# Optimization experiments

Measured on AMD Instinct MI355X. Metric: run time of the kernel, lower is better.

Reference implementation:

```python
import jax, jax.numpy as jnp
import numpy as np

B, N, D_IN = 8, 1024, 512
H, D_HEAD = 8, 64
D_EXPAND, D_OUT = 2048, 512
D_Q = D_HEAD * H            # 512
D_V = D_IN * H              # 4096
D_QKV = 2 * D_Q + D_V       # 5120
EPS = 1e-5


def setup_inputs() -> dict:
    key = jax.random.key(0)
    ks = jax.random.split(key, 16)
    s = 0.02
    return {
        "x": jax.random.normal(ks[0], (B, N, D_IN), jnp.float32),
        "pos_enc": jax.random.normal(ks[1], (1, N, D_IN), jnp.float32),
        "gamma1": jnp.ones((1, 1, D_IN), jnp.float32),
        "beta1": jnp.zeros((1, 1, D_IN), jnp.float32),
        "scale": jnp.asarray(1.414, jnp.float32),
        "W_qkv": jax.random.normal(ks[2], (D_IN, D_QKV), jnp.float32) * s,
        "b_qkv": jax.random.normal(ks[3], (D_QKV,), jnp.float32) * s,
        "W_merge": jax.random.normal(ks[4], (D_V, D_IN), jnp.float32) * s,
        "b_merge": jax.random.normal(ks[5], (D_IN,), jnp.float32) * s,
        "gamma2": jnp.ones((1, 1, D_IN), jnp.float32),
        "beta2": jnp.zeros((1, 1, D_IN), jnp.float32),
        "W1": jax.random.normal(ks[6], (D_IN, D_EXPAND), jnp.float32) * s,
        "b1": jax.random.normal(ks[7], (D_EXPAND,), jnp.float32) * s,
        "gamma3": jnp.ones((1, 1, D_EXPAND), jnp.float32),
        "beta3": jnp.zeros((1, 1, D_EXPAND), jnp.float32),
        "W2": jax.random.normal(ks[8], (D_EXPAND, D_OUT), jnp.float32) * s,
        "b2": jax.random.normal(ks[9], (D_OUT,), jnp.float32) * s,
    }


def _feature_norm(x, gamma, beta):
    # torch FeatureNorm: stats over dim=1 (sequence dim), unbiased=False
    mean = x.mean(axis=1, keepdims=True)
    var = x.var(axis=1, keepdims=True)
    return gamma * (x - mean) / jnp.sqrt(var + EPS) + beta


def _swish(x):
    return x * jax.nn.sigmoid(x)


def reference(x, pos_enc, gamma1, beta1, scale, W_qkv, b_qkv, W_merge, b_merge,
              gamma2, beta2, W1, b1, gamma3, beta3, W2, b2):
    Bs, Ns, _ = x.shape
    h = _feature_norm(x, gamma1, beta1) + pos_enc
    qkv = _swish(h) @ W_qkv + b_qkv                      # (B, N, D_QKV)
    q = qkv[..., :D_Q].reshape(Bs, Ns, H, D_HEAD).transpose(0, 2, 1, 3)        # (B,H,N,dh)
    k = qkv[..., D_Q:2 * D_Q].reshape(Bs, Ns, H, D_HEAD).transpose(0, 2, 1, 3)
    v = qkv[..., 2 * D_Q:].reshape(Bs, Ns, H, D_IN).transpose(0, 2, 1, 3)      # (B,H,N,d_in)
    # squared euclidean distance via |q|^2 + |k|^2 - 2 q.k
    q2 = jnp.sum(q * q, axis=-1)                         # (B,H,N)
    k2 = jnp.sum(k * k, axis=-1)                         # (B,H,N)
    qk = jnp.einsum('bhnc,bhmc->bhnm', q, k)             # (B,H,N,N)
    d2 = jnp.maximum(q2[..., :, None] + k2[..., None, :] - 2.0 * qk, 0.0)
    score = jnp.exp(-d2 / (scale * scale))               # RBF kernel, no softmax
    out = jnp.einsum('bhnm,bhmc->bhnc', score, v)        # (B,H,N,d_in)
    out = out.transpose(0, 2, 1, 3).reshape(Bs, Ns, H * D_IN)
    x2 = x + out @ W_merge + b_merge                     # merge heads + residual
    ffh = _feature_norm(x2, gamma2, beta2) @ W1 + b1
    ffh = _swish(_feature_norm(ffh, gamma3, beta3))
    ff = ffh @ W2 + b2
    return ff + x2                                        # shortcut is Identity (d_in == d_out)
```

## Files before the change

### kernel.cpp

```cpp
#include <hip/hip_runtime.h>
#include <hip/hip_bf16.h>
#include <stdint.h>

typedef __bf16 bf16_t;
typedef __bf16 bf16x8 __attribute__((ext_vector_type(8)));
typedef __bf16 bf16x4 __attribute__((ext_vector_type(4)));
typedef float f32x4 __attribute__((ext_vector_type(4)));

__global__ void transp_kernel(const float* __restrict__ in, bf16_t* __restrict__ out,
                              int K, int N) {
  __shared__ float tile[32][33];
  int k0 = blockIdx.x * 32, n0 = blockIdx.y * 32;
  int tx = threadIdx.x, ty = threadIdx.y;
#pragma unroll
  for (int i = 0; i < 4; i++)
    tile[ty + 8 * i][tx] = in[(size_t)(k0 + ty + 8 * i) * N + n0 + tx];
  __syncthreads();
#pragma unroll
  for (int i = 0; i < 4; i++)
    out[(size_t)(n0 + ty + 8 * i) * K + k0 + tx] = (bf16_t)tile[tx][ty + 8 * i];
}

#define NSPLIT 16

__global__ __launch_bounds__(256) void norm_partial(
    const float* __restrict__ in, float* __restrict__ part, int D) {
  const int nd = D >> 7;
  const int bid = blockIdx.x;
  const int s = bid % NSPLIT;
  const int rem = bid / NSPLIT;
  const int dc = rem % nd;
  const int b = rem / nd;
  const int t = threadIdx.x;
  const int d = (dc << 7) + (t & 127);
  const int half = t >> 7;
  const int rows = 1024 / NSPLIT;
  const float* base = in + ((size_t)b * 1024 + s * rows) * D + d;
  float sum = 0.f, sq = 0.f;
  for (int n = half; n < rows; n += 2) {
    float v = base[(size_t)n * D];
    sum += v;
    sq += v * v;
  }
  __shared__ float r0[256], r1[256];
  r0[t] = sum;
  r1[t] = sq;
  __syncthreads();
  if (t < 128) {
    float ssum = r0[t] + r0[t + 128];
    float ssq = r1[t] + r1[t + 128];
    size_t col = (size_t)b * D + (dc << 7) + t;
    part[col * (2 * NSPLIT) + s] = ssum;
    part[col * (2 * NSPLIT) + NSPLIT + s] = ssq;
  }
}

__global__ __launch_bounds__(256) void norm_stats(
    const float* __restrict__ part, float2* __restrict__ stats, int total) {
  int col = blockIdx.x * 256 + threadIdx.x;
  if (col >= total) return;
  const float* p = part + (size_t)col * (2 * NSPLIT);
  float sum = 0.f, sq = 0.f;
#pragma unroll
  for (int s = 0; s < NSPLIT; s++) {
    sum += p[s];
    sq += p[NSPLIT + s];
  }
  float mean = sum * (1.f / 1024.f);
  float var = sq * (1.f / 1024.f) - mean * mean;
  stats[col] = make_float2(mean, rsqrtf(var + 1e-5f));
}

template <int MODE>
__global__ __launch_bounds__(256) void norm_apply(
    const float* __restrict__ in, const float2* __restrict__ stats,
    const float* __restrict__ gamma, const float* __restrict__ beta,
    const float* __restrict__ pos, bf16_t* __restrict__ out, int logD) {
  const int D = 1 << logD;
  size_t idx = ((size_t)blockIdx.x * 256 + threadIdx.x) * 4;
  int d = (int)(idx & (D - 1));
  size_t row = idx >> logD;
  int b = (int)(row >> 10);
  int n = (int)(row & 1023);
  float4 v = *(const float4*)(in + idx);
  float4 g = *(const float4*)(gamma + d);
  float4 be = *(const float4*)(beta + d);
  const float2* st = stats + (size_t)b * D + d;
  float vv[4] = {v.x, v.y, v.z, v.w};
  float gg[4] = {g.x, g.y, g.z, g.w};
  float bb[4] = {be.x, be.y, be.z, be.w};
  float pp[4] = {0.f, 0.f, 0.f, 0.f};
  if (MODE == 1) {
    float4 p = *(const float4*)(pos + (size_t)n * D + d);
    pp[0] = p.x; pp[1] = p.y; pp[2] = p.z; pp[3] = p.w;
  }
  bf16x4 o;
#pragma unroll
  for (int j = 0; j < 4; j++) {
    float2 s = st[j];
    float h = gg[j] * (vv[j] - s.x) * s.y + bb[j];
    if (MODE == 1) h += pp[j];
    if (MODE == 1 || MODE == 3) h = h / (1.f + __expf(-h));
    o[j] = (bf16_t)h;
  }
  *(bf16x4*)(out + idx) = o;
}

enum { EPI_QKV = 0, EPI_F32 = 1, EPI_F32RES = 2 };

template <int EPI>
__global__ void __launch_bounds__(256, 2) gemm_bf16(
    const bf16_t* __restrict__ A, const bf16_t* __restrict__ Bt,
    const float* __restrict__ bias, const float* __restrict__ res,
    void* __restrict__ out0, bf16_t* __restrict__ out1,
    int M, int N, int K) {
  __shared__ bf16_t smem[2 * 128 * 64];
  bf16_t* sA = smem;
  bf16_t* sB = smem + 128 * 64;
  const int mt = M >> 7;
  const int bm = blockIdx.x % mt;
  const int bn = blockIdx.x / mt;
  const int t = threadIdx.x;
  const int w = t >> 6, l = t & 63;
  const int wm = w >> 1, wn = w & 1;
  const int lrow = l >> 3;
  const int lcol = (l & 7) ^ lrow;

  f32x4 acc[4][4];
  const f32x4 z4 = {0.f, 0.f, 0.f, 0.f};
#pragma unroll
  for (int m = 0; m < 4; m++)
#pragma unroll
    for (int n = 0; n < 4; n++) acc[m][n] = z4;

  const bf16_t* Asrc = A + (size_t)(bm * 128 + w * 32 + lrow) * K + lcol * 8;
  const bf16_t* Bsrc = Bt + (size_t)(bn * 128 + w * 32 + lrow) * K + lcol * 8;

  for (int kk = 0; kk < K; kk += 64) {
#pragma unroll
    for (int i = 0; i < 4; i++) {
      __builtin_amdgcn_global_load_lds(
          (const __attribute__((address_space(1))) void*)(const void*)(Asrc + (size_t)i * 8 * K + kk),
          (__attribute__((address_space(3))) void*)(void*)((char*)sA + (w * 4 + i) * 1024),
          16, 0, 0);
      __builtin_amdgcn_global_load_lds(
          (const __attribute__((address_space(1))) void*)(const void*)(Bsrc + (size_t)i * 8 * K + kk),
          (__attribute__((address_space(3))) void*)(void*)((char*)sB + (w * 4 + i) * 1024),
          16, 0, 0);
    }
    __syncthreads();
#pragma unroll
    for (int ks = 0; ks < 2; ks++) {
      bf16x8 af[4], bfr[4];
      const int lc = ks * 4 + (l >> 4);
#pragma unroll
      for (int m = 0; m < 4; m++) {
        int row = wm * 64 + m * 16 + (l & 15);
        af[m] = *(const bf16x8*)((const char*)sA + row * 128 + ((lc ^ (row & 7)) << 4));
      }
#pragma unroll
      for (int n = 0; n < 4; n++) {
        int row = wn * 64 + n * 16 + (l & 15);
        bfr[n] = *(const bf16x8*)((const char*)sB + row * 128 + ((lc ^ (row & 7)) << 4));
      }
#pragma unroll
      for (int m = 0; m < 4; m++)
#pragma unroll
        for (int n = 0; n < 4; n++)
          acc[m][n] = __builtin_amdgcn_mfma_f32_16x16x32_bf16(af[m], bfr[n], acc[m][n], 0, 0, 0);
    }
    __syncthreads();
  }

  const int rowbase = bm * 128 + wm * 64 + ((l >> 4) << 2);
  const int colbase = bn * 128 + wn * 64 + (l & 15);
#pragma unroll
  for (int m = 0; m < 4; m++) {
#pragma unroll
    for (int n = 0; n < 4; n++) {
      int row = rowbase + m * 16;
      int col = colbase + n * 16;
      float bc = bias[col];
      if (EPI == EPI_QKV) {
        if (col < 1024) {
          bf16_t* qkb = (bf16_t*)out0;
#pragma unroll
          for (int r = 0; r < 4; r++)
            qkb[(size_t)(row + r) * 1024 + col] = (bf16_t)(acc[m][n][r] + bc);
        } else {
          int c2 = col - 1024;
          int hh = c2 >> 9, vc = c2 & 511;
          int bidx = row >> 10, nidx = row & 1023;
          bf16x4 pk;
#pragma unroll
          for (int r = 0; r < 4; r++) pk[r] = (bf16_t)(acc[m][n][r] + bc);
          *(bf16x4*)(out1 + ((size_t)((bidx << 3) + hh) * 512 + vc) * 1024 + nidx) = pk;
        }
      } else {
        float* o = (float*)out0;
#pragma unroll
        for (int r = 0; r < 4; r++) {
          float v = acc[m][n][r] + bc;
          if (EPI == EPI_F32RES) v += res[(size_t)(row + r) * N + col];
          o[(size_t)(row + r) * N + col] = v;
        }
      }
    }
  }
}

__global__ void q2k2_kernel(const bf16_t* __restrict__ qk, float* __restrict__ q2,
                            float* __restrict__ k2) {
  int tid = blockIdx.x * 256 + threadIdx.x;
  int b = tid >> 13;
  int h = (tid >> 10) & 7;
  int n = tid & 1023;
  const bf16_t* row = qk + (size_t)((b << 10) + n) * 1024 + (h << 6);
  float sq = 0.f, sk = 0.f;
#pragma unroll
  for (int i = 0; i < 8; i++) {
    bf16x8 vq = *(const bf16x8*)(row + i * 8);
    bf16x8 vk = *(const bf16x8*)(row + 512 + i * 8);
#pragma unroll
    for (int j = 0; j < 8; j++) {
      float fq = (float)vq[j];
      sq += fq * fq;
      float fk = (float)vk[j];
      sk += fk * fk;
    }
  }
  q2[tid] = sq;
  k2[tid] = sk;
}

__global__ void __launch_bounds__(256, 2) attn_kernel(
    const bf16_t* __restrict__ qk, const bf16_t* __restrict__ vt,
    const float* __restrict__ q2, const float* __restrict__ k2,
    const float* __restrict__ scale_p, bf16_t* __restrict__ attn_out) {
  __shared__ bf16_t s_lds[64 * 64];
  const int blk = blockIdx.x;
  const int mtile = blk & 15;
  const int bh = blk >> 4;
  const int b = bh >> 3, h = bh & 7;
  const int t = threadIdx.x, w = t >> 6, l = t & 63;
  const float sc = scale_p[0];
  const float minus_inv = -1.f / (sc * sc);

  const bf16_t* qbase = qk + ((size_t)((b << 10) + (mtile << 6))) * 1024 + (h << 6);
  bf16x8 qf[4][2];
#pragma unroll
  for (int it = 0; it < 4; it++)
#pragma unroll
    for (int kc = 0; kc < 2; kc++)
      qf[it][kc] = *(const bf16x8*)(qbase + (size_t)(it * 16 + (l & 15)) * 1024 +
                                    kc * 32 + ((l >> 4) << 3));
  float q2r[4];
  const float* q2base = q2 + (bh << 10) + (mtile << 6);
#pragma unroll
  for (int it = 0; it < 4; it++) q2r[it] = q2base[it * 16 + (l & 15)];

  f32x4 acc[4][8];
  const f32x4 z4 = {0.f, 0.f, 0.f, 0.f};
#pragma unroll
  for (int m = 0; m < 4; m++)
#pragma unroll
    for (int nn = 0; nn < 8; nn++) acc[m][nn] = z4;

  const bf16_t* kbase = qk + ((size_t)(b << 10)) * 1024 + 512 + (h << 6);
  const bf16_t* vbase = vt + ((size_t)(bh << 9)) * 1024;
  const float* k2base = k2 + (bh << 10);

  for (int kt = 0; kt < 16; kt++) {
    float k2r[4];
#pragma unroll
    for (int r = 0; r < 4; r++)
      k2r[r] = k2base[kt * 64 + w * 16 + ((l >> 4) << 2) + r];
    f32x4 sacc[4];
#pragma unroll
    for (int it = 0; it < 4; it++) sacc[it] = z4;
#pragma unroll
    for (int kc = 0; kc < 2; kc++) {
      bf16x8 kf = *(const bf16x8*)(kbase + (size_t)(kt * 64 + w * 16 + (l & 15)) * 1024 +
                                   kc * 32 + ((l >> 4) << 3));
#pragma unroll
      for (int it = 0; it < 4; it++)
        sacc[it] = __builtin_amdgcn_mfma_f32_16x16x32_bf16(kf, qf[it][kc], sacc[it], 0, 0, 0);
    }
    __syncthreads();
#pragma unroll
    for (int it = 0; it < 4; it++) {
      int i = it * 16 + (l & 15);
      bf16x4 pk;
#pragma unroll
      for (int r = 0; r < 4; r++) {
        float d2 = fmaxf(q2r[it] + k2r[r] - 2.f * sacc[it][r], 0.f);
        pk[r] = (bf16_t)__expf(d2 * minus_inv);
      }
      int jc8 = (w << 2) + (l >> 4);
      *(bf16x4*)((char*)s_lds + i * 128 + ((jc8 ^ ((i & 7) << 1)) << 3)) = pk;
    }
    __syncthreads();
#pragma unroll
    for (int kc = 0; kc < 2; kc++) {
      bf16x8 sf[4];
#pragma unroll
      for (int m = 0; m < 4; m++) {
        int i = m * 16 + (l & 15);
        int jcA = (kc << 3) + ((l >> 4) << 1);
        sf[m] = *(const bf16x8*)((const char*)s_lds + i * 128 +
                                 ((jcA ^ ((i & 7) << 1)) << 3));
      }
#pragma unroll
      for (int nn = 0; nn < 8; nn++) {
        bf16x8 vf = *(const bf16x8*)(vbase + (size_t)(w * 128 + nn * 16 + (l & 15)) * 1024 +
                                     kt * 64 + (kc << 5) + ((l >> 4) << 3));
#pragma unroll
        for (int m = 0; m < 4; m++)
          acc[m][nn] = __builtin_amdgcn_mfma_f32_16x16x32_bf16(sf[m], vf, acc[m][nn], 0, 0, 0);
      }
    }
  }
#pragma unroll
  for (int m = 0; m < 4; m++) {
    int nidx = (mtile << 6) + m * 16 + ((l >> 4) << 2);
#pragma unroll
    for (int nn = 0; nn < 8; nn++) {
      int col = (h << 9) + w * 128 + nn * 16 + (l & 15);
      bf16_t* o = attn_out + ((size_t)((b << 10) + nidx)) * 4096 + col;
#pragma unroll
      for (int r = 0; r < 4; r++) o[(size_t)r * 4096] = (bf16_t)acc[m][nn][r];
    }
  }
}

extern "C" void kernel_launch(void* const* d_in, const int* in_sizes, int n_in,
                              void* d_out, int out_size, void* d_ws, size_t ws_size,
                              hipStream_t stream) {
  const float* x    = (const float*)d_in[0];
  const float* pos  = (const float*)d_in[1];
  const float* g1   = (const float*)d_in[2];
  const float* be1  = (const float*)d_in[3];
  const float* scl  = (const float*)d_in[4];
  const float* Wqkv = (const float*)d_in[5];
  const float* bqkv = (const float*)d_in[6];
  const float* Wmrg = (const float*)d_in[7];
  const float* bmrg = (const float*)d_in[8];
  const float* g2   = (const float*)d_in[9];
  const float* be2  = (const float*)d_in[10];
  const float* W1   = (const float*)d_in[11];
  const float* b1   = (const float*)d_in[12];
  const float* g3   = (const float*)d_in[13];
  const float* be3  = (const float*)d_in[14];
  const float* W2   = (const float*)d_in[15];
  const float* b2   = (const float*)d_in[16];
  float* outp = (float*)d_out;

  char* ws = (char*)d_ws;
  size_t off = 0;
  auto alloc = [&](size_t bytes) {
    char* p = ws + off;
    off += (bytes + 255) & ~(size_t)255;
    return p;
  };
  bf16_t* wtq = (bf16_t*)alloc(5120ull * 512 * 2);
  bf16_t* wtm = (bf16_t*)alloc(512ull * 4096 * 2);
  bf16_t* wt1 = (bf16_t*)alloc(2048ull * 512 * 2);
  bf16_t* wt2 = (bf16_t*)alloc(512ull * 2048 * 2);
  float*  q2  = (float*)alloc(65536ull * 4);
  float*  k2  = (float*)alloc(65536ull * 4);
  float*  prt = (float*)alloc(16384ull * 2 * NSPLIT * 4);
  float2* sts = (float2*)alloc(16384ull * 8);
  bf16_t* swh = (bf16_t*)alloc(8192ull * 512 * 2);
  bf16_t* qkb = (bf16_t*)alloc(8192ull * 1024 * 2);
  float*  x2b = (float*)alloc(8192ull * 512 * 4);
  bf16_t* x2n = (bf16_t*)alloc(8192ull * 512 * 2);
  bf16_t* atn = (bf16_t*)alloc(8192ull * 4096 * 2);
  bf16_t* vtb = (bf16_t*)alloc(64ull * 512 * 1024 * 2);
  float*  ffh = (float*)vtb;
  bf16_t* ffn = (bf16_t*)atn;

  dim3 tb(32, 8);
  transp_kernel<<<dim3(512 / 32, 5120 / 32), tb, 0, stream>>>(Wqkv, wtq, 512, 5120);
  transp_kernel<<<dim3(4096 / 32, 512 / 32), tb, 0, stream>>>(Wmrg, wtm, 4096, 512);
  transp_kernel<<<dim3(512 / 32, 2048 / 32), tb, 0, stream>>>(W1, wt1, 512, 2048);
  transp_kernel<<<dim3(2048 / 32, 512 / 32), tb, 0, stream>>>(W2, wt2, 2048, 512);

  norm_partial<<<8 * 4 * NSPLIT, 256, 0, stream>>>(x, prt, 512);
  norm_stats<<<16, 256, 0, stream>>>(prt, sts, 8 * 512);
  norm_apply<1><<<4096, 256, 0, stream>>>(x, sts, g1, be1, pos, swh, 9);

  gemm_bf16<EPI_QKV><<<64 * 40, 256, 0, stream>>>(swh, wtq, bqkv, nullptr,
                                                  (void*)qkb, vtb, 8192, 5120, 512);
  q2k2_kernel<<<256, 256, 0, stream>>>(qkb, q2, k2);
  attn_kernel<<<1024, 256, 0, stream>>>(qkb, vtb, q2, k2, scl, atn);
  gemm_bf16<EPI_F32RES><<<64 * 4, 256, 0, stream>>>(atn, wtm, bmrg, x,
                                                    (void*)x2b, nullptr, 8192, 512, 4096);

  norm_partial<<<8 * 4 * NSPLIT, 256, 0, stream>>>(x2b, prt, 512);
  norm_stats<<<16, 256, 0, stream>>>(prt, sts, 8 * 512);
  norm_apply<2><<<4096, 256, 0, stream>>>(x2b, sts, g2, be2, nullptr, x2n, 9);

  gemm_bf16<EPI_F32><<<64 * 16, 256, 0, stream>>>(x2n, wt1, b1, nullptr,
                                                  (void*)ffh, nullptr, 8192, 2048, 512);

  norm_partial<<<8 * 16 * NSPLIT, 256, 0, stream>>>(ffh, prt, 2048);
  norm_stats<<<64, 256, 0, stream>>>(prt, sts, 8 * 2048);
  norm_apply<3><<<16384, 256, 0, stream>>>(ffh, sts, g3, be3, nullptr, ffn, 11);

  gemm_bf16<EPI_F32RES><<<64 * 4, 256, 0, stream>>>(ffn, wt2, b2, x2b,
                                                    (void*)outp, nullptr, 8192, 512, 2048);
}
```

Measured before the change: 544.8 us.

## Split-K the narrow GEMMs, bf16 FFN hidden, larger attention blocks, XCD swizzle

The two N=512 GEMMs (merge and W2) are split into two K halves, doubling the workgroup count, and a new combine kernel sums the partials with bias and residual. The FFN hidden activation is stored in bf16 instead of fp32, with the norm kernels templated to read bf16. The attention kernel now uses 512 threads covering 128 query rows per block and preloads V fragments before its MFMAs. The GEMM workgroup index is remapped in groups of 8, apparently to spread neighbouring tiles across the chip's compute dies. In exchange, split-K adds fp32 partial writes plus an extra pass, and bf16 storage of the hidden lowers precision before the norm.

```diff
diff --git a/kernel.cpp b/kernel.cpp
--- a/kernel.cpp
+++ b/kernel.cpp
@@ -23,8 +23,9 @@
 
 #define NSPLIT 16
 
+template <typename T>
 __global__ __launch_bounds__(256) void norm_partial(
-    const float* __restrict__ in, float* __restrict__ part, int D) {
+    const T* __restrict__ in, float* __restrict__ part, int D) {
   const int nd = D >> 7;
   const int bid = blockIdx.x;
   const int s = bid % NSPLIT;
@@ -35,10 +36,10 @@
   const int d = (dc << 7) + (t & 127);
   const int half = t >> 7;
   const int rows = 1024 / NSPLIT;
-  const float* base = in + ((size_t)b * 1024 + s * rows) * D + d;
+  const T* base = in + ((size_t)b * 1024 + s * rows) * D + d;
   float sum = 0.f, sq = 0.f;
   for (int n = half; n < rows; n += 2) {
-    float v = base[(size_t)n * D];
+    float v = (float)base[(size_t)n * D];
     sum += v;
     sq += v * v;
   }
@@ -71,9 +72,9 @@
   stats[col] = make_float2(mean, rsqrtf(var + 1e-5f));
 }
 
-template <int MODE>
+template <int MODE, typename T>
 __global__ __launch_bounds__(256) void norm_apply(
-    const float* __restrict__ in, const float2* __restrict__ stats,
+    const T* __restrict__ in, const float2* __restrict__ stats,
     const float* __restrict__ gamma, const float* __restrict__ beta,
     const float* __restrict__ pos, bf16_t* __restrict__ out, int logD) {
   const int D = 1 << logD;
@@ -82,11 +83,18 @@
   size_t row = idx >> logD;
   int b = (int)(row >> 10);
   int n = (int)(row & 1023);
-  float4 v = *(const float4*)(in + idx);
+  float vv[4];
+  if constexpr (sizeof(T) == 4) {
+    float4 v = *(const float4*)(in + idx);
+    vv[0] = v.x; vv[1] = v.y; vv[2] = v.z; vv[3] = v.w;
+  } else {
+    bf16x4 v = *(const bf16x4*)(in + idx);
+#pragma unroll
+    for (int j = 0; j < 4; j++) vv[j] = (float)v[j];
+  }
   float4 g = *(const float4*)(gamma + d);
   float4 be = *(const float4*)(beta + d);
   const float2* st = stats + (size_t)b * D + d;
-  float vv[4] = {v.x, v.y, v.z, v.w};
   float gg[4] = {g.x, g.y, g.z, g.w};
   float bb[4] = {be.x, be.y, be.z, be.w};
   float pp[4] = {0.f, 0.f, 0.f, 0.f};
@@ -106,20 +114,47 @@
   *(bf16x4*)(out + idx) = o;
 }
 
-enum { EPI_QKV = 0, EPI_F32 = 1, EPI_F32RES = 2 };
-
-template <int EPI>
+__global__ __launch_bounds__(256) void combine2(
+    const float* __restrict__ p0, const float* __restrict__ p1,
+    const float* __restrict__ bias, const float* __restrict__ res,
+    float* __restrict__ out) {
+  size_t idx = ((size_t)blockIdx.x * 256 + threadIdx.x) * 4;
+  int col = (int)(idx & 511);
+  float4 a = *(const float4*)(p0 + idx);
+  float4 b = *(const float4*)(p1 + idx);
+  float4 rr = *(const float4*)(res + idx);
+  float4 bi = *(const float4*)(bias + col);
+  float4 o;
+  o.x = a.x + b.x + rr.x + bi.x;
+  o.y = a.y + b.y + rr.y + bi.y;
+  o.z = a.z + b.z + rr.z + bi.z;
+  o.w = a.w + b.w + rr.w + bi.w;
+  *(float4*)(out + idx) = o;
+}
+
+enum { EPI_QKV = 0, EPI_RAW = 1, EPI_BF16 = 2 };
+
+template <int EPI, int SPLITK>
 __global__ void __launch_bounds__(256, 2) gemm_bf16(
     const bf16_t* __restrict__ A, const bf16_t* __restrict__ Bt,
-    const float* __restrict__ bias, const float* __restrict__ res,
+    const float* __restrict__ bias,
     void* __restrict__ out0, bf16_t* __restrict__ out1,
     int M, int N, int K) {
   __shared__ bf16_t smem[2 * 128 * 64];
   bf16_t* sA = smem;
   bf16_t* sB = smem + 128 * 64;
+  const int nwg = gridDim.x;
+  int wg = blockIdx.x;
+  wg = (wg & 7) * (nwg >> 3) + (wg >> 3);
+  int kslice = 0;
+  if (SPLITK) {
+    int half = nwg >> 1;
+    kslice = (wg >= half) ? 1 : 0;
+    wg -= kslice * half;
+  }
   const int mt = M >> 7;
-  const int bm = blockIdx.x % mt;
-  const int bn = blockIdx.x / mt;
+  const int bm = wg % mt;
+  const int bn = wg / mt;
   const int t = threadIdx.x;
   const int w = t >> 6, l = t & 63;
   const int wm = w >> 1, wn = w & 1;
@@ -136,7 +171,9 @@
   const bf16_t* Asrc = A + (size_t)(bm * 128 + w * 32 + lrow) * K + lcol * 8;
   const bf16_t* Bsrc = Bt + (size_t)(bn * 128 + w * 32 + lrow) * K + lcol * 8;
 
-  for (int kk = 0; kk < K; kk += 64) {
+  const int kbeg = SPLITK ? kslice * (K >> 1) : 0;
+  const int kend = kbeg + (SPLITK ? (K >> 1) : K);
+  for (int kk = kbeg; kk < kend; kk += 64) {
 #pragma unroll
     for (int i = 0; i < 4; i++) {
       __builtin_amdgcn_global_load_lds(
@@ -180,8 +217,8 @@
     for (int n = 0; n < 4; n++) {
       int row = rowbase + m * 16;
       int col = colbase + n * 16;
-      float bc = bias[col];
       if (EPI == EPI_QKV) {
+        float bc = bias[col];
         if (col < 1024) {
           bf16_t* qkb = (bf16_t*)out0;
 #pragma unroll
@@ -196,14 +233,15 @@
           for (int r = 0; r < 4; r++) pk[r] = (bf16_t)(acc[m][n][r] + bc);
           *(bf16x4*)(out1 + ((size_t)((bidx << 3) + hh) * 512 + vc) * 1024 + nidx) = pk;
         }
+      } else if (EPI == EPI_RAW) {
+        float* o = (float*)out0 + (size_t)kslice * M * N;
+#pragma unroll
+        for (int r = 0; r < 4; r++) o[(size_t)(row + r) * N + col] = acc[m][n][r];
       } else {
-        float* o = (float*)out0;
-#pragma unroll
-        for (int r = 0; r < 4; r++) {
-          float v = acc[m][n][r] + bc;
-          if (EPI == EPI_F32RES) v += res[(size_t)(row + r) * N + col];
-          o[(size_t)(row + r) * N + col] = v;
-        }
+        float bc = bias[col];
+#pragma unroll
+        for (int r = 0; r < 4; r++)
+          out1[(size_t)(row + r) * N + col] = (bf16_t)(acc[m][n][r] + bc);
       }
     }
   }
@@ -233,20 +271,23 @@
   k2[tid] = sk;
 }
 
-__global__ void __launch_bounds__(256, 2) attn_kernel(
+__global__ void __launch_bounds__(512, 4) attn_kernel(
     const bf16_t* __restrict__ qk, const bf16_t* __restrict__ vt,
     const float* __restrict__ q2, const float* __restrict__ k2,
     const float* __restrict__ scale_p, bf16_t* __restrict__ attn_out) {
-  __shared__ bf16_t s_lds[64 * 64];
+  __shared__ bf16_t s_lds[128 * 64];
   const int blk = blockIdx.x;
-  const int mtile = blk & 15;
-  const int bh = blk >> 4;
+  const int bh = (blk & 7) * 8 + (blk >> 6);
+  const int mtile = (blk >> 3) & 7;
   const int b = bh >> 3, h = bh & 7;
   const int t = threadIdx.x, w = t >> 6, l = t & 63;
+  const int wq = w >> 2;
+  const int wv = w & 3;
   const float sc = scale_p[0];
   const float minus_inv = -1.f / (sc * sc);
 
-  const bf16_t* qbase = qk + ((size_t)((b << 10) + (mtile << 6))) * 1024 + (h << 6);
+  const bf16_t* qbase =
+      qk + ((size_t)((b << 10) + (mtile << 7) + (wq << 6))) * 1024 + (h << 6);
   bf16x8 qf[4][2];
 #pragma unroll
   for (int it = 0; it < 4; it++)
@@ -255,7 +296,7 @@
       qf[it][kc] = *(const bf16x8*)(qbase + (size_t)(it * 16 + (l & 15)) * 1024 +
                                     kc * 32 + ((l >> 4) << 3));
   float q2r[4];
-  const float* q2base = q2 + (bh << 10) + (mtile << 6);
+  const float* q2base = q2 + (bh << 10) + (mtile << 7) + (wq << 6);
 #pragma unroll
   for (int it = 0; it < 4; it++) q2r[it] = q2base[it * 16 + (l & 15)];
 
@@ -274,13 +315,13 @@
     float k2r[4];
 #pragma unroll
     for (int r = 0; r < 4; r++)
-      k2r[r] = k2base[kt * 64 + w * 16 + ((l >> 4) << 2) + r];
+      k2r[r] = k2base[kt * 64 + wv * 16 + ((l >> 4) << 2) + r];
     f32x4 sacc[4];
 #pragma unroll
     for (int it = 0; it < 4; it++) sacc[it] = z4;
 #pragma unroll
     for (int kc = 0; kc < 2; kc++) {
-      bf16x8 kf = *(const bf16x8*)(kbase + (size_t)(kt * 64 + w * 16 + (l & 15)) * 1024 +
+      bf16x8 kf = *(const bf16x8*)(kbase + (size_t)(kt * 64 + wv * 16 + (l & 15)) * 1024 +
                                    kc * 32 + ((l >> 4) << 3));
 #pragma unroll
       for (int it = 0; it < 4; it++)
@@ -289,14 +330,14 @@
     __syncthreads();
 #pragma unroll
     for (int it = 0; it < 4; it++) {
-      int i = it * 16 + (l & 15);
+      int i = (wq << 6) + it * 16 + (l & 15);
       bf16x4 pk;
 #pragma unroll
       for (int r = 0; r < 4; r++) {
         float d2 = fmaxf(q2r[it] + k2r[r] - 2.f * sacc[it][r], 0.f);
         pk[r] = (bf16_t)__expf(d2 * minus_inv);
       }
-      int jc8 = (w << 2) + (l >> 4);
+      int jc8 = (wv << 2) + (l >> 4);
       *(bf16x4*)((char*)s_lds + i * 128 + ((jc8 ^ ((i & 7) << 1)) << 3)) = pk;
     }
     __syncthreads();
@@ -305,27 +346,29 @@
       bf16x8 sf[4];
 #pragma unroll
       for (int m = 0; m < 4; m++) {
-        int i = m * 16 + (l & 15);
+        int i = (wq << 6) + m * 16 + (l & 15);
         int jcA = (kc << 3) + ((l >> 4) << 1);
         sf[m] = *(const bf16x8*)((const char*)s_lds + i * 128 +
                                  ((jcA ^ ((i & 7) << 1)) << 3));
       }
-#pragma unroll
-      for (int nn = 0; nn < 8; nn++) {
-        bf16x8 vf = *(const bf16x8*)(vbase + (size_t)(w * 128 + nn * 16 + (l & 15)) * 1024 +
-                                     kt * 64 + (kc << 5) + ((l >> 4) << 3));
+      bf16x8 vf[8];
+#pragma unroll
+      for (int nn = 0; nn < 8; nn++)
+        vf[nn] = *(const bf16x8*)(vbase + (size_t)(wv * 128 + nn * 16 + (l & 15)) * 1024 +
+                                  kt * 64 + (kc << 5) + ((l >> 4) << 3));
+#pragma unroll
+      for (int nn = 0; nn < 8; nn++)
 #pragma unroll
         for (int m = 0; m < 4; m++)
-          acc[m][nn] = __builtin_amdgcn_mfma_f32_16x16x32_bf16(sf[m], vf, acc[m][nn], 0, 0, 0);
-      }
+          acc[m][nn] = __builtin_amdgcn_mfma_f32_16x16x32_bf16(sf[m], vf[nn], acc[m][nn], 0, 0, 0);
     }
   }
 #pragma unroll
   for (int m = 0; m < 4; m++) {
-    int nidx = (mtile << 6) + m * 16 + ((l >> 4) << 2);
+    int nidx = (mtile << 7) + (wq << 6) + m * 16 + ((l >> 4) << 2);
 #pragma unroll
     for (int nn = 0; nn < 8; nn++) {
-      int col = (h << 9) + w * 128 + nn * 16 + (l & 15);
+      int col = (h << 9) + wv * 128 + nn * 16 + (l & 15);
       bf16_t* o = attn_out + ((size_t)((b << 10) + nidx)) * 4096 + col;
 #pragma unroll
       for (int r = 0; r < 4; r++) o[(size_t)r * 4096] = (bf16_t)acc[m][nn][r];
@@ -376,7 +419,9 @@
   bf16_t* x2n = (bf16_t*)alloc(8192ull * 512 * 2);
   bf16_t* atn = (bf16_t*)alloc(8192ull * 4096 * 2);
   bf16_t* vtb = (bf16_t*)alloc(64ull * 512 * 1024 * 2);
-  float*  ffh = (float*)vtb;
+  float*  pmg = (float*)vtb;
+  bf16_t* ffh = (bf16_t*)vtb;
+  float*  pff = (float*)(vtb + 8192ull * 2048);
   bf16_t* ffn = (bf16_t*)atn;
 
   dim3 tb(32, 8);
@@ -385,28 +430,31 @@
   transp_kernel<<<dim3(512 / 32, 2048 / 32), tb, 0, stream>>>(W1, wt1, 512, 2048);
   transp_kernel<<<dim3(2048 / 32, 512 / 32), tb, 0, stream>>>(W2, wt2, 2048, 512);
 
-  norm_partial<<<8 * 4 * NSPLIT, 256, 0, stream>>>(x, prt, 512);
+  norm_partial<float><<<8 * 4 * NSPLIT, 256, 0, stream>>>(x, prt, 512);
   norm_stats<<<16, 256, 0, stream>>>(prt, sts, 8 * 512);
-  norm_apply<1><<<4096, 256, 0, stream>>>(x, sts, g1, be1, pos, swh, 9);
-
-  gemm_bf16<EPI_QKV><<<64 * 40, 256, 0, stream>>>(swh, wtq, bqkv, nullptr,
-                                                  (void*)qkb, vtb, 8192, 5120, 512);
+  norm_apply<1, float><<<4096, 256, 0, stream>>>(x, sts, g1, be1, pos, swh, 9);
+
+  gemm_bf16<EPI_QKV, 0><<<64 * 40, 256, 0, stream>>>(swh, wtq, bqkv,
+                                                     (void*)qkb, vtb, 8192, 5120, 512);
   q2k2_kernel<<<256, 256, 0, stream>>>(qkb, q2, k2);
-  attn_kernel<<<1024, 256, 0, stream>>>(qkb, vtb, q2, k2, scl, atn);
-  gemm_bf16<EPI_F32RES><<<64 * 4, 256, 0, stream>>>(atn, wtm, bmrg, x,
-                                                    (void*)x2b, nullptr, 8192, 512, 4096);
-
-  norm_partial<<<8 * 4 * NSPLIT, 256, 0, stream>>>(x2b, prt, 512);
+  attn_kernel<<<512, 512, 0, stream>>>(qkb, vtb, q2, k2, scl, atn);
+
+  gemm_bf16<EPI_RAW, 1><<<2 * 64 * 4, 256, 0, stream>>>(atn, wtm, nullptr,
+                                                        (void*)pmg, nullptr, 8192, 512, 4096);
+  combine2<<<4096, 256, 0, stream>>>(pmg, pmg + 8192ull * 512, bmrg, x, x2b);
+
+  norm_partial<float><<<8 * 4 * NSPLIT, 256, 0, stream>>>(x2b, prt, 512);
   norm_stats<<<16, 256, 0, stream>>>(prt, sts, 8 * 512);
-  norm_apply<2><<<4096, 256, 0, stream>>>(x2b, sts, g2, be2, nullptr, x2n, 9);
-
-  gemm_bf16<EPI_F32><<<64 * 16, 256, 0, stream>>>(x2n, wt1, b1, nullptr,
-                                                  (void*)ffh, nullptr, 8192, 2048, 512);
-
-  norm_partial<<<8 * 16 * NSPLIT, 256, 0, stream>>>(ffh, prt, 2048);
+  norm_apply<2, float><<<4096, 256, 0, stream>>>(x2b, sts, g2, be2, nullptr, x2n, 9);
+
+  gemm_bf16<EPI_BF16, 0><<<64 * 16, 256, 0, stream>>>(x2n, wt1, b1,
+                                                      nullptr, ffh, 8192, 2048, 512);
+
+  norm_partial<bf16_t><<<8 * 16 * NSPLIT, 256, 0, stream>>>(ffh, prt, 2048);
   norm_stats<<<64, 256, 0, stream>>>(prt, sts, 8 * 2048);
-  norm_apply<3><<<16384, 256, 0, stream>>>(ffh, sts, g3, be3, nullptr, ffn, 11);
-
-  gemm_bf16<EPI_F32RES><<<64 * 4, 256, 0, stream>>>(ffn, wt2, b2, x2b,
-                                                    (void*)outp, nullptr, 8192, 512, 2048);
-}
+  norm_apply<3, bf16_t><<<16384, 256, 0, stream>>>(ffh, sts, g3, be3, nullptr, ffn, 11);
+
+  gemm_bf16<EPI_RAW, 1><<<2 * 64 * 4, 256, 0, stream>>>(ffn, wt2, nullptr,
+                                                        (void*)pff, nullptr, 8192, 512, 2048);
+  combine2<<<4096, 256, 0, stream>>>(pff, pff + 8192ull * 512, b2, x2b, outp);
+}
```

After: 1.197 ms. 120% more time.
